# Optimization experiments

Hardware: AMD Instinct MI355X
Metric: run time of the kernel (lower is better)

## Reference

```python
import jax, jax.numpy as jnp
import numpy as np

EPS = 1e-5
B, CIN, L = 512, 5, 1024   # batch, input channels, msp length == d_model
COUT, A, NB = 32, 13, 5    # CNN branch channels, max_atoms, num_bonds_prediction


def conv1d(x, w, pad, groups=1):
    # x: (N, C, L), w: (O, I/groups, K)
    return jax.lax.conv_general_dilated(
        x, w, window_strides=(1,), padding=[(pad, pad)],
        dimension_numbers=("NCH", "OIH", "NCH"), feature_group_count=groups)


def batchnorm(x, g, b):
    # training-mode BN over (N, L) per channel, as nn.BatchNorm1d in train()
    m = jnp.mean(x, axis=(0, 2), keepdims=True)
    v = jnp.var(x, axis=(0, 2), keepdims=True)
    return (x - m) * jax.lax.rsqrt(v + EPS) * g[None, :, None] + b[None, :, None]


def setup_inputs() -> dict:
    key = jax.random.key(0)
    ks = jax.random.split(key, 16)
    n = jax.random.normal
    inp = {
        "src": n(ks[0], (B, CIN, L), dtype=jnp.float32),
        "mask": jnp.ones((B, A), dtype=bool),
        "max_atoms": A,
        # CNN branch 1 (kernel 5) : depthwise, pointwise, BN, residual 1x1 conv
        "dw1": n(ks[1], (CIN, 1, 5), dtype=jnp.float32) * 0.2,
        "pw1": n(ks[2], (COUT, CIN, 1), dtype=jnp.float32) * 0.2,
        "g1": jnp.ones((COUT,), jnp.float32),
        "be1": jnp.zeros((COUT,), jnp.float32),
        "r1w": n(ks[3], (COUT, CIN, 1), dtype=jnp.float32) * 0.2,
        "r1b": jnp.zeros((COUT,), jnp.float32),
        # CNN branch 2 (kernel 3)
        "dw2": n(ks[4], (CIN, 1, 3), dtype=jnp.float32) * 0.2,
        "pw2": n(ks[5], (COUT, CIN, 1), dtype=jnp.float32) * 0.2,
        "g2": jnp.ones((COUT,), jnp.float32),
        "be2": jnp.zeros((COUT,), jnp.float32),
        "r2w": n(ks[6], (COUT, CIN, 1), dtype=jnp.float32) * 0.2,
        "r2b": jnp.zeros((COUT,), jnp.float32),
        # EdgeClassify2 linears: ll1 (2*COUT -> A), fl (2*L -> NB)
        "ll1w": n(ks[7], (A, 2 * COUT), dtype=jnp.float32) * 0.1,
        "ll1b": jnp.zeros((A,), jnp.float32),
        "flw": n(ks[8], (NB, 2 * L), dtype=jnp.float32) * 0.02,
        "flb": jnp.zeros((NB,), jnp.float32),
    }
    return inp


def reference(src, mask, max_atoms, dw1, pw1, g1, be1, r1w, r1b,
              dw2, pw2, g2, be2, r2w, r2b, ll1w, ll1b, flw, flb):
    # ---- CNN encoder ----
    e1 = jax.nn.relu(batchnorm(conv1d(conv1d(src, dw1, 2, groups=CIN), pw1, 0), g1, be1))
    e1 = e1 * (conv1d(src, r1w, 0) + r1b[None, :, None])
    e2 = jax.nn.relu(batchnorm(conv1d(conv1d(src, dw2, 1, groups=CIN), pw2, 0), g2, be2))
    e2 = e2 * (conv1d(src, r2w, 0) + r2b[None, :, None])
    x = jnp.concatenate([e1, e2], axis=1)          # (B, 2*COUT, L)
    # ---- EdgeClassify2 ----
    # ll1 over channel dim: (B, 2*COUT, L) -> (B, A, L)
    h = jnp.einsum("bcl,ac->bal", x, ll1w) + ll1b[None, :, None]
    # vectorized replacement of the O(A^2) python loop:
    # final_e[:, i, j] = concat(h[:, min(i,j)], h[:, max(i,j)])
    idx = jnp.arange(max_atoms)
    mn = jnp.minimum(idx[:, None], idx[None, :])   # (A, A)
    mx = jnp.maximum(idx[:, None], idx[None, :])
    final_e = jnp.concatenate([h[:, mn, :], h[:, mx, :]], axis=-1)  # (B, A, A, 2L)
    out = jnp.einsum("bijd,nd->bijn", final_e, flw) + flb           # (B, A, A, NB)
    return out
```

## Files before the change

### kernel.cpp

```cpp
#include <hip/hip_runtime.h>
#include <hip/hip_bf16.h>

#define BB 512
#define LL 1024
#define AA 13
#define NBP 5
#define NTOT (BB * LL)
#define EPSV 1e-5f

#define WS_F     192
#define WS_PART  256
#define WS_CONST 10496
#define WS_S     16384

typedef __attribute__((ext_vector_type(8))) short bhalf8;
typedef __attribute__((ext_vector_type(4))) float floatx4;

__device__ __forceinline__ unsigned int pk_bf16(float a, float b) {
    __hip_bfloat162 h = __float22bfloat162_rn(make_float2(a, b));
    union { __hip_bfloat162 h2; unsigned int u; } cv; cv.h2 = h;
    return cv.u;
}

template<int CTRL, int RM, bool BC>
__device__ __forceinline__ float dppadd(float v) {
    int t = __builtin_amdgcn_update_dpp(0, __float_as_int(v), CTRL, RM, 0xf, BC);
    return v + __int_as_float(t);
}
__device__ __forceinline__ float wave_sum(float v) {
    v = dppadd<0x111, 0xf, true >(v);
    v = dppadd<0x112, 0xf, true >(v);
    v = dppadd<0x114, 0xf, true >(v);
    v = dppadd<0x118, 0xf, true >(v);
    v = dppadd<0x142, 0xa, false>(v);
    v = dppadd<0x143, 0xc, false>(v);
    return v;
}

__global__ __launch_bounds__(256) void k_moments(
    const float* __restrict__ src,
    const float* __restrict__ dw1,
    const float* __restrict__ dw2,
    const float* __restrict__ flw,
    float* __restrict__ ws)
{
    __shared__ float red[4][40];
    __shared__ float fred[4];
    int tid = threadIdx.x;
    int gid = blockIdx.x * 256 + tid;
    int b = gid >> 7, L0 = (gid & 127) << 3;
    const float* sb = src + b * (5 * LL);

    float w1[5][5], w2[5][3];
#pragma unroll
    for (int c = 0; c < 5; c++) {
#pragma unroll
        for (int t = 0; t < 5; t++) w1[c][t] = dw1[c*5+t];
#pragma unroll
        for (int t = 0; t < 3; t++) w2[c][t] = dw2[c*3+t];
    }

    float x[5][16];
#pragma unroll
    for (int c5 = 0; c5 < 5; c5++) {
        const float* sp = sb + c5 * LL;
        float4 xa = (L0 >= 4)    ? *(const float4*)(sp + L0 - 4) : make_float4(0,0,0,0);
        float4 xb = *(const float4*)(sp + L0);
        float4 xc = *(const float4*)(sp + L0 + 4);
        float4 xd = (L0 <= 1012) ? *(const float4*)(sp + L0 + 8) : make_float4(0,0,0,0);
        x[c5][0]=xa.x; x[c5][1]=xa.y; x[c5][2]=xa.z; x[c5][3]=xa.w;
        x[c5][4]=xb.x; x[c5][5]=xb.y; x[c5][6]=xb.z; x[c5][7]=xb.w;
        x[c5][8]=xc.x; x[c5][9]=xc.y; x[c5][10]=xc.z; x[c5][11]=xc.w;
        x[c5][12]=xd.x; x[c5][13]=xd.y; x[c5][14]=xd.z; x[c5][15]=xd.w;
    }

    float acc[40];
#pragma unroll
    for (int k = 0; k < 40; k++) acc[k] = 0.f;

#pragma unroll
    for (int k = 0; k < 8; k++) {
        float d1[5], d2[5];
#pragma unroll
        for (int c5 = 0; c5 < 5; c5++) {
            d1[c5] = w1[c5][0]*x[c5][k+2] + w1[c5][1]*x[c5][k+3] + w1[c5][2]*x[c5][k+4]
                   + w1[c5][3]*x[c5][k+5] + w1[c5][4]*x[c5][k+6];
            d2[c5] = w2[c5][0]*x[c5][k+3] + w2[c5][1]*x[c5][k+4] + w2[c5][2]*x[c5][k+5];
        }
#pragma unroll
        for (int j = 0; j < 5; j++) { acc[j] += d1[j]; acc[20+j] += d2[j]; }
#pragma unroll
        for (int j = 0; j < 5; j++)
#pragma unroll
            for (int kk = j; kk < 5; kk++) {
                int idx = j*(11-j)/2 + (kk - j);
                acc[5+idx]  += d1[j]*d1[kk];
                acc[25+idx] += d2[j]*d2[kk];
            }
    }

    int lane = tid & 63, wv = tid >> 6;
#pragma unroll
    for (int k = 0; k < 40; k++) acc[k] = wave_sum(acc[k]);
    if (lane == 63) {
#pragma unroll
        for (int k = 0; k < 40; k++) red[wv][k] = acc[k];
    }
    __syncthreads();
    if (tid < 40) {
        ws[WS_PART + blockIdx.x * 40 + tid] =
            red[0][tid] + red[1][tid] + red[2][tid] + red[3][tid];
    }

    if (blockIdx.x < 10) {
        int nn = blockIdx.x;
        int n = nn < 5 ? nn : nn - 5;
        int off = nn < 5 ? 0 : LL;
        float4 v = *(const float4*)(flw + n * (2*LL) + off + tid * 4);
        float s = wave_sum(v.x + v.y + v.z + v.w);
        if (lane == 63) fred[wv] = s;
        __syncthreads();
        if (tid == 0) ws[WS_F + nn] = fred[0] + fred[1] + fred[2] + fred[3];
    }
}

__global__ __launch_bounds__(320) void k_prep(
    float* __restrict__ ws,
    const float* __restrict__ pw1, const float* __restrict__ pw2,
    const float* __restrict__ g1,  const float* __restrict__ be1,
    const float* __restrict__ g2,  const float* __restrict__ be2,
    const float* __restrict__ r1w, const float* __restrict__ r2w,
    const float* __restrict__ r1b, const float* __restrict__ r2b)
{
    __shared__ float momS[40];
    int tid = threadIdx.x;
    {
        int k = tid >> 3, sub = tid & 7;
        float v = 0.f;
#pragma unroll 8
        for (int t2 = 0; t2 < 32; t2++) v += ws[WS_PART + (sub + (t2 << 3)) * 40 + k];
        v += __shfl_xor(v, 1, 64);
        v += __shfl_xor(v, 2, 64);
        v += __shfl_xor(v, 4, 64);
        if (sub == 0) momS[k] = v;
    }
    __syncthreads();
    if (tid < 64) {
        int brc = tid >> 5, o = tid & 31;
        const float invN = 1.0f / (float)NTOT;
        const float* pw = brc ? pw2 : pw1;
        const float* rw = brc ? r2w : r1w;
        const float* s  = momS + (brc ? 20 : 0);
        const float* M  = momS + (brc ? 25 : 5);
        float pwv[5], rwv[5], md[5];
#pragma unroll
        for (int j = 0; j < 5; j++) { pwv[j] = pw[o*5+j]; rwv[j] = rw[o*5+j]; md[j] = s[j] * invN; }
        float meanY = 0.f;
#pragma unroll
        for (int j = 0; j < 5; j++) meanY += pwv[j] * md[j];
        float ey2 = 0.f;
#pragma unroll
        for (int j = 0; j < 5; j++)
#pragma unroll
            for (int k = 0; k < 5; k++) {
                int lo = j < k ? j : k, hi = j < k ? k : j;
                int idx = lo*(11-lo)/2 + (hi - lo);
                ey2 += pwv[j] * pwv[k] * (M[idx] * invN);
            }
        float varY = ey2 - meanY * meanY;
        if (varY < 0.f) varY = 0.f;
        float gg = brc ? g2[o] : g1[o];
        float bb = brc ? be2[o] : be1[o];
        float rb = brc ? r2b[o] : r1b[o];
        float sc = gg * rsqrtf(varY + EPSV);
        float sh = bb - meanY * sc;
        float* dst = ws + WS_CONST + tid * 16;
        dst[0] = pwv[0]*sc; dst[1] = pwv[1]*sc; dst[2] = pwv[2]*sc; dst[3] = pwv[3]*sc;
        dst[4] = pwv[4]*sc; dst[5] = sh;        dst[6] = rb;        dst[7] = 0.f;
        dst[8] = rwv[0];    dst[9] = rwv[1];    dst[10] = rwv[2];   dst[11] = rwv[3];
        dst[12] = rwv[4];   dst[13] = 0.f;      dst[14] = 0.f;      dst[15] = 0.f;
    }
}

__global__ __launch_bounds__(512, 4) void k_fused(
    const float* __restrict__ src,
    const float* __restrict__ dw1,
    const float* __restrict__ dw2,
    const float* __restrict__ flw,
    const float* __restrict__ ws_ro,
    float* __restrict__ ws)
{
    __shared__ __align__(16) unsigned int eBuf[8192];

    int tid = threadIdx.x, bb = blockIdx.x;
    int b = bb >> 1, h = bb & 1;
    int lane = tid & 63;
    int gu = __builtin_amdgcn_readfirstlane(tid >> 6);
    int br = gu >> 2;
    int c0 = gu << 3;

    const float* srcB = src + b * (5 * LL);

    float wdw[5][5];
    if (br == 0) {
#pragma unroll
        for (int c5 = 0; c5 < 5; c5++)
#pragma unroll
            for (int t = 0; t < 5; t++) wdw[c5][t] = dw1[c5*5+t];
    } else {
#pragma unroll
        for (int c5 = 0; c5 < 5; c5++) {
            wdw[c5][0] = 0.f;
            wdw[c5][1] = dw2[c5*3+0]; wdw[c5][2] = dw2[c5*3+1]; wdw[c5][3] = dw2[c5*3+2];
            wdw[c5][4] = 0.f;
        }
    }
    const float* cb = ws_ro + WS_CONST + (c0 << 4);

    int mt   = gu & 3;
    int kgrp = gu >> 2;
    floatx4 Cacc = {0.f, 0.f, 0.f, 0.f};

    int nB = lane & 15;
    int kg = (lane >> 4) << 3;
    const float* fbase = flw + (nB % 5) * 2048 + (nB / 5) * 1024;

    char* eb = (char*)eBuf;

#pragma unroll 1
    for (int p = 0; p < 4; ++p) {
        float fv[2][8];
        {
            int gl0 = (h << 9) + (p << 7) + (kgrp << 6) + kg;
            if (nB < 10) {
                float4 a0 = *(const float4*)(fbase + gl0);
                float4 a1 = *(const float4*)(fbase + gl0 + 4);
                float4 b0 = *(const float4*)(fbase + gl0 + 32);
                float4 b1 = *(const float4*)(fbase + gl0 + 36);
                fv[0][0]=a0.x; fv[0][1]=a0.y; fv[0][2]=a0.z; fv[0][3]=a0.w;
                fv[0][4]=a1.x; fv[0][5]=a1.y; fv[0][6]=a1.z; fv[0][7]=a1.w;
                fv[1][0]=b0.x; fv[1][1]=b0.y; fv[1][2]=b0.z; fv[1][3]=b0.w;
                fv[1][4]=b1.x; fv[1][5]=b1.y; fv[1][6]=b1.z; fv[1][7]=b1.w;
            } else {
#pragma unroll
                for (int j = 0; j < 8; j++) { fv[0][j] = 0.f; fv[1][j] = 0.f; }
            }
        }

        int l0 = (h << 9) + (p << 7) + (lane << 1);
        float dv[5][2], sv[5][2];
#pragma unroll
        for (int c5 = 0; c5 < 5; c5++) {
            const float* s5 = srcB + (c5 << 10);
            float2 xa = (l0 >= 2)    ? *(const float2*)(s5 + l0 - 2) : make_float2(0.f, 0.f);
            float2 xb = *(const float2*)(s5 + l0);
            float2 xc = (l0 <= 1020) ? *(const float2*)(s5 + l0 + 2) : make_float2(0.f, 0.f);
            float xx[6] = {xa.x, xa.y, xb.x, xb.y, xc.x, xc.y};
            sv[c5][0] = xb.x; sv[c5][1] = xb.y;
            if (br == 0) {
#pragma unroll
                for (int q = 0; q < 2; q++)
                    dv[c5][q] = wdw[c5][0]*xx[q] + wdw[c5][1]*xx[q+1] + wdw[c5][2]*xx[q+2]
                              + wdw[c5][3]*xx[q+3] + wdw[c5][4]*xx[q+4];
            } else {
#pragma unroll
                for (int q = 0; q < 2; q++)
                    dv[c5][q] = wdw[c5][1]*xx[q+1] + wdw[c5][2]*xx[q+2] + wdw[c5][3]*xx[q+3];
            }
        }

        int wcol = lane << 2;
#pragma unroll
        for (int ci = 0; ci < 8; ci++) {
            const float4 A  = *(const float4*)(cb + ci*16);
            const float4 B2 = *(const float4*)(cb + ci*16 + 4);
            const float4 R0 = *(const float4*)(cb + ci*16 + 8);
            const float4 R1 = *(const float4*)(cb + ci*16 + 12);
            float e[2];
#pragma unroll
            for (int q = 0; q < 2; q++) {
                float y = B2.y + A.x*dv[0][q] + A.y*dv[1][q] + A.z*dv[2][q]
                                + A.w*dv[3][q] + B2.x*dv[4][q];
                float r = B2.z + R0.x*sv[0][q] + R0.y*sv[1][q] + R0.z*sv[2][q]
                                + R0.w*sv[3][q] + R1.x*sv[4][q];
                e[q] = fmaxf(y, 0.f) * r;
            }
            unsigned int hp = pk_bf16(e[0], e[1]);
            float hi0 = __uint_as_float(hp << 16);
            float hi1 = __uint_as_float(hp & 0xFFFF0000u);
            unsigned int lp = pk_bf16(e[0] - hi0, e[1] - hi1);
            int c = c0 + ci;
            int off = (c << 8) + (wcol ^ ((c & 7) << 4));
            *(unsigned int*)(eb + off)         = hp;
            *(unsigned int*)(eb + 16384 + off) = lp;
        }
        __syncthreads();

        {
            int arow = (mt << 4) + (lane & 15);
            int swz  = (arow & 7) << 4;
            int rb2  = arow << 8;
            bhalf8 bH[2], bL[2];
#pragma unroll
            for (int kk = 0; kk < 2; kk++) {
                union { unsigned int u[4]; bhalf8 v; } uh, ul;
#pragma unroll
                for (int j = 0; j < 4; j++) {
                    float f0 = fv[kk][2*j], f1 = fv[kk][2*j+1];
                    unsigned int hp = pk_bf16(f0, f1);
                    float hi0 = __uint_as_float(hp << 16);
                    float hi1 = __uint_as_float(hp & 0xFFFF0000u);
                    uh.u[j] = hp;
                    ul.u[j] = pk_bf16(f0 - hi0, f1 - hi1);
                }
                bH[kk] = uh.v; bL[kk] = ul.v;
            }
#pragma unroll
            for (int kk = 0; kk < 2; kk++) {
                int kbyte = (((kgrp << 6) + (kk << 5) + kg) << 1) ^ swz;
                bhalf8 aH = *(const bhalf8*)(eb + rb2 + kbyte);
                bhalf8 aL = *(const bhalf8*)(eb + 16384 + rb2 + kbyte);
                Cacc = __builtin_amdgcn_mfma_f32_16x16x32_bf16(aH, bH[kk], Cacc, 0, 0, 0);
                Cacc = __builtin_amdgcn_mfma_f32_16x16x32_bf16(aH, bL[kk], Cacc, 0, 0, 0);
                Cacc = __builtin_amdgcn_mfma_f32_16x16x32_bf16(aL, bH[kk], Cacc, 0, 0, 0);
            }
        }
        __syncthreads();
    }

    {
        float* part = (float*)eBuf;
        int basep = (gu << 8) + ((lane >> 4) << 6) + (lane & 15);
        part[basep]      = Cacc[0];
        part[basep + 16] = Cacc[1];
        part[basep + 32] = Cacc[2];
        part[basep + 48] = Cacc[3];
    }
    __syncthreads();
    for (int idx = tid; idx < 640; idx += 512) {
        int c = idx / 10, n = idx - c * 10;
        int mt2 = c >> 4, row = c & 15;
        const float* part = (const float*)eBuf;
        int o = (row << 4) + n;
        ws[WS_S + bb * 640 + idx] = part[mt2 * 256 + o] + part[(4 + mt2) * 256 + o];
    }
}

__global__ __launch_bounds__(256) void k_out(
    const float* __restrict__ ws,
    const float* __restrict__ ll1w,
    const float* __restrict__ ll1b,
    const float* __restrict__ flb,
    float* __restrict__ out)
{
    __shared__ float llT[832];
    __shared__ float S[640];
    __shared__ float PQ[130];

    int tid = threadIdx.x, b = blockIdx.x;
    for (int idx = tid; idx < 832; idx += 256) {
        int cc = idx / 13, a = idx - cc * 13;
        llT[idx] = ll1w[a * 64 + cc];
    }
    const float* s0 = ws + WS_S + (b * 2) * 640;
    const float* s1 = ws + WS_S + (b * 2 + 1) * 640;
    for (int idx = tid; idx < 640; idx += 256) S[idx] = s0[idx] + s1[idx];
    __syncthreads();

    if (tid < 130) {
        int half = tid >= 65 ? 1 : 0;
        int q = tid - half * 65;
        int a = q / 5, n = q - a * 5;
        int col = half * 5 + n;
        float v = ll1b[a] * ws[WS_F + col];
#pragma unroll 8
        for (int cc = 0; cc < 64; cc++) v += llT[cc * 13 + a] * S[cc * 10 + col];
        PQ[tid] = v;
    }
    __syncthreads();

    for (int idx = tid; idx < AA * AA * NBP; idx += 256) {
        int i = idx / 65;
        int rr = idx - i * 65;
        int j = rr / 5, n = rr - j * 5;
        int mn = i < j ? i : j, mx = i < j ? j : i;
        out[b * (AA * AA * NBP) + idx] = PQ[mn * 5 + n] + PQ[65 + mx * 5 + n] + flb[n];
    }
}

extern "C" void kernel_launch(void* const* d_in, const int* in_sizes, int n_in,
                              void* d_out, int out_size, void* d_ws, size_t ws_size,
                              hipStream_t stream) {
    const float* src  = (const float*)d_in[0];
    const float* dw1  = (const float*)d_in[3];
    const float* pw1  = (const float*)d_in[4];
    const float* g1   = (const float*)d_in[5];
    const float* be1  = (const float*)d_in[6];
    const float* r1w  = (const float*)d_in[7];
    const float* r1b  = (const float*)d_in[8];
    const float* dw2  = (const float*)d_in[9];
    const float* pw2  = (const float*)d_in[10];
    const float* g2   = (const float*)d_in[11];
    const float* be2  = (const float*)d_in[12];
    const float* r2w  = (const float*)d_in[13];
    const float* r2b  = (const float*)d_in[14];
    const float* ll1w = (const float*)d_in[15];
    const float* ll1b = (const float*)d_in[16];
    const float* flw  = (const float*)d_in[17];
    const float* flb  = (const float*)d_in[18];
    float* ws  = (float*)d_ws;
    float* out = (float*)d_out;

    k_moments<<<256, 256, 0, stream>>>(src, dw1, dw2, flw, ws);
    k_prep<<<1, 320, 0, stream>>>(ws, pw1, pw2, g1, be1, g2, be2, r1w, r2w, r1b, r2b);
    k_fused<<<BB * 2, 512, 0, stream>>>(src, dw1, dw2, flw, ws, ws);
    k_out<<<BB, 256, 0, stream>>>(ws, ll1w, ll1b, flb, out);
}
```

Baseline: 157.5 us.

## Precompute depthwise conv once into LDS and build MFMA A-operands in registers

The fused kernel now computes both depthwise conv outputs and the source samples once per position into a swizzled shared buffer, behind a single barrier. Each wave then builds its bf16 hi/lo A fragments directly in registers from that buffer, one channel per lane, instead of staging the elementwise products through shared memory with two barriers per iteration. Per-channel constants are loaded once rather than per iteration. In exchange, each lane does eight positions of pointwise work per step with more shared-memory reads, and the work is split differently across waves.

Measured after the change: 142.1 us. -9.8%, faster.

```diff
diff --git a/kernel.cpp b/kernel.cpp
--- a/kernel.cpp
+++ b/kernel.cpp
@@ -190,146 +190,103 @@
     const float* __restrict__ ws_ro,
     float* __restrict__ ws)
 {
-    __shared__ __align__(16) unsigned int eBuf[8192];
+    __shared__ __align__(16) float dvS[9216 + 64];
 
     int tid = threadIdx.x, bb = blockIdx.x;
     int b = bb >> 1, h = bb & 1;
     int lane = tid & 63;
     int gu = __builtin_amdgcn_readfirstlane(tid >> 6);
-    int br = gu >> 2;
-    int c0 = gu << 3;
+    int mt = gu & 3, lq = gu >> 2;
+    int br = mt >> 1;
 
     const float* srcB = src + b * (5 * LL);
-
-    float wdw[5][5];
-    if (br == 0) {
-#pragma unroll
-        for (int c5 = 0; c5 < 5; c5++)
-#pragma unroll
-            for (int t = 0; t < 5; t++) wdw[c5][t] = dw1[c5*5+t];
-    } else {
+    char* base  = (char*)dvS;
+    char* cbase = (char*)(dvS + 8192);
+
+    {
+        int t = tid, lg = (h << 9) + t;
+        int swz = ((t >> 3) & 3) << 4;
+        float d1v[5], d2v[5], s0[5];
 #pragma unroll
         for (int c5 = 0; c5 < 5; c5++) {
-            wdw[c5][0] = 0.f;
-            wdw[c5][1] = dw2[c5*3+0]; wdw[c5][2] = dw2[c5*3+1]; wdw[c5][3] = dw2[c5*3+2];
-            wdw[c5][4] = 0.f;
-        }
-    }
-    const float* cb = ws_ro + WS_CONST + (c0 << 4);
-
-    int mt   = gu & 3;
-    int kgrp = gu >> 2;
-    floatx4 Cacc = {0.f, 0.f, 0.f, 0.f};
+            const float* s5 = srcB + (c5 << 10);
+            float xm2 = (lg >= 2)    ? s5[lg - 2] : 0.f;
+            float xm1 = (lg >= 1)    ? s5[lg - 1] : 0.f;
+            float x0  = s5[lg];
+            float xp1 = (lg <= 1022) ? s5[lg + 1] : 0.f;
+            float xp2 = (lg <= 1021) ? s5[lg + 2] : 0.f;
+            d1v[c5] = dw1[c5*5+0]*xm2 + dw1[c5*5+1]*xm1 + dw1[c5*5+2]*x0
+                    + dw1[c5*5+3]*xp1 + dw1[c5*5+4]*xp2;
+            d2v[c5] = dw2[c5*3+0]*xm1 + dw2[c5*3+1]*x0 + dw2[c5*3+2]*xp1;
+            s0[c5] = x0;
+        }
+        *(float4*)(base + ((((0<<10)+(t<<1)+0) << 4) ^ swz)) = make_float4(d1v[0],d1v[1],d1v[2],d1v[3]);
+        *(float4*)(base + ((((0<<10)+(t<<1)+1) << 4) ^ swz)) = make_float4(d1v[4],s0[0],s0[1],s0[2]);
+        *(float4*)(base + ((((1<<10)+(t<<1)+0) << 4) ^ swz)) = make_float4(d2v[0],d2v[1],d2v[2],d2v[3]);
+        *(float4*)(base + ((((1<<10)+(t<<1)+1) << 4) ^ swz)) = make_float4(d2v[4],s0[0],s0[1],s0[2]);
+        *(float2*)(cbase + (t << 3)) = make_float2(s0[3], s0[4]);
+    }
+    __syncthreads();
+
+    int ch = (mt << 4) + (lane & 15);
+    const float* cf = ws_ro + WS_CONST + (ch << 4);
+    const float4 A  = *(const float4*)cf;
+    const float4 B2 = *(const float4*)(cf + 4);
+    const float4 R0 = *(const float4*)(cf + 8);
+    const float r4w = cf[12];
 
     int nB = lane & 15;
     int kg = (lane >> 4) << 3;
     const float* fbase = flw + (nB % 5) * 2048 + (nB / 5) * 1024;
-
-    char* eb = (char*)eBuf;
+    floatx4 Cacc = {0.f, 0.f, 0.f, 0.f};
 
 #pragma unroll 1
-    for (int p = 0; p < 4; ++p) {
-        float fv[2][8];
-        {
-            int gl0 = (h << 9) + (p << 7) + (kgrp << 6) + kg;
-            if (nB < 10) {
-                float4 a0 = *(const float4*)(fbase + gl0);
-                float4 a1 = *(const float4*)(fbase + gl0 + 4);
-                float4 b0 = *(const float4*)(fbase + gl0 + 32);
-                float4 b1 = *(const float4*)(fbase + gl0 + 36);
-                fv[0][0]=a0.x; fv[0][1]=a0.y; fv[0][2]=a0.z; fv[0][3]=a0.w;
-                fv[0][4]=a1.x; fv[0][5]=a1.y; fv[0][6]=a1.z; fv[0][7]=a1.w;
-                fv[1][0]=b0.x; fv[1][1]=b0.y; fv[1][2]=b0.z; fv[1][3]=b0.w;
-                fv[1][4]=b1.x; fv[1][5]=b1.y; fv[1][6]=b1.z; fv[1][7]=b1.w;
-            } else {
-#pragma unroll
-                for (int j = 0; j < 8; j++) { fv[0][j] = 0.f; fv[1][j] = 0.f; }
-            }
-        }
-
-        int l0 = (h << 9) + (p << 7) + (lane << 1);
-        float dv[5][2], sv[5][2];
-#pragma unroll
-        for (int c5 = 0; c5 < 5; c5++) {
-            const float* s5 = srcB + (c5 << 10);
-            float2 xa = (l0 >= 2)    ? *(const float2*)(s5 + l0 - 2) : make_float2(0.f, 0.f);
-            float2 xb = *(const float2*)(s5 + l0);
-            float2 xc = (l0 <= 1020) ? *(const float2*)(s5 + l0 + 2) : make_float2(0.f, 0.f);
-            float xx[6] = {xa.x, xa.y, xb.x, xb.y, xc.x, xc.y};
-            sv[c5][0] = xb.x; sv[c5][1] = xb.y;
-            if (br == 0) {
-#pragma unroll
-                for (int q = 0; q < 2; q++)
-                    dv[c5][q] = wdw[c5][0]*xx[q] + wdw[c5][1]*xx[q+1] + wdw[c5][2]*xx[q+2]
-                              + wdw[c5][3]*xx[q+3] + wdw[c5][4]*xx[q+4];
-            } else {
-#pragma unroll
-                for (int q = 0; q < 2; q++)
-                    dv[c5][q] = wdw[c5][1]*xx[q+1] + wdw[c5][2]*xx[q+2] + wdw[c5][3]*xx[q+3];
-            }
-        }
-
-        int wcol = lane << 2;
-#pragma unroll
-        for (int ci = 0; ci < 8; ci++) {
-            const float4 A  = *(const float4*)(cb + ci*16);
-            const float4 B2 = *(const float4*)(cb + ci*16 + 4);
-            const float4 R0 = *(const float4*)(cb + ci*16 + 8);
-            const float4 R1 = *(const float4*)(cb + ci*16 + 12);
-            float e[2];
-#pragma unroll
-            for (int q = 0; q < 2; q++) {
-                float y = B2.y + A.x*dv[0][q] + A.y*dv[1][q] + A.z*dv[2][q]
-                                + A.w*dv[3][q] + B2.x*dv[4][q];
-                float r = B2.z + R0.x*sv[0][q] + R0.y*sv[1][q] + R0.z*sv[2][q]
-                                + R0.w*sv[3][q] + R1.x*sv[4][q];
-                e[q] = fmaxf(y, 0.f) * r;
-            }
-            unsigned int hp = pk_bf16(e[0], e[1]);
+    for (int s = 0; s < 8; ++s) {
+        int lb = (lq << 8) + (s << 5) + kg;
+        float4 f0 = make_float4(0,0,0,0), f1 = make_float4(0,0,0,0);
+        if (nB < 10) {
+            f0 = *(const float4*)(fbase + (h << 9) + lb);
+            f1 = *(const float4*)(fbase + (h << 9) + lb + 4);
+        }
+        int sw = ((lb >> 3) & 3) << 4;
+        float e[8];
+#pragma unroll
+        for (int i = 0; i < 8; ++i) {
+            int l = lb + i;
+            const float4 pa = *(const float4*)(base + ((((br<<10)+(l<<1)+0) << 4) ^ sw));
+            const float4 pb = *(const float4*)(base + ((((br<<10)+(l<<1)+1) << 4) ^ sw));
+            const float2 pc = *(const float2*)(cbase + (l << 3));
+            float y = B2.y + A.x*pa.x + A.y*pa.y + A.z*pa.z + A.w*pa.w + B2.x*pb.x;
+            float r = B2.z + R0.x*pb.y + R0.y*pb.z + R0.z*pb.w + R0.w*pc.x + r4w*pc.y;
+            e[i] = fmaxf(y, 0.f) * r;
+        }
+        union { unsigned int u[4]; bhalf8 v; } ah, al;
+#pragma unroll
+        for (int j = 0; j < 4; j++) {
+            unsigned int hp = pk_bf16(e[2*j], e[2*j+1]);
             float hi0 = __uint_as_float(hp << 16);
             float hi1 = __uint_as_float(hp & 0xFFFF0000u);
-            unsigned int lp = pk_bf16(e[0] - hi0, e[1] - hi1);
-            int c = c0 + ci;
-            int off = (c << 8) + (wcol ^ ((c & 7) << 4));
-            *(unsigned int*)(eb + off)         = hp;
-            *(unsigned int*)(eb + 16384 + off) = lp;
-        }
-        __syncthreads();
-
-        {
-            int arow = (mt << 4) + (lane & 15);
-            int swz  = (arow & 7) << 4;
-            int rb2  = arow << 8;
-            bhalf8 bH[2], bL[2];
-#pragma unroll
-            for (int kk = 0; kk < 2; kk++) {
-                union { unsigned int u[4]; bhalf8 v; } uh, ul;
-#pragma unroll
-                for (int j = 0; j < 4; j++) {
-                    float f0 = fv[kk][2*j], f1 = fv[kk][2*j+1];
-                    unsigned int hp = pk_bf16(f0, f1);
-                    float hi0 = __uint_as_float(hp << 16);
-                    float hi1 = __uint_as_float(hp & 0xFFFF0000u);
-                    uh.u[j] = hp;
-                    ul.u[j] = pk_bf16(f0 - hi0, f1 - hi1);
-                }
-                bH[kk] = uh.v; bL[kk] = ul.v;
-            }
-#pragma unroll
-            for (int kk = 0; kk < 2; kk++) {
-                int kbyte = (((kgrp << 6) + (kk << 5) + kg) << 1) ^ swz;
-                bhalf8 aH = *(const bhalf8*)(eb + rb2 + kbyte);
-                bhalf8 aL = *(const bhalf8*)(eb + 16384 + rb2 + kbyte);
-                Cacc = __builtin_amdgcn_mfma_f32_16x16x32_bf16(aH, bH[kk], Cacc, 0, 0, 0);
-                Cacc = __builtin_amdgcn_mfma_f32_16x16x32_bf16(aH, bL[kk], Cacc, 0, 0, 0);
-                Cacc = __builtin_amdgcn_mfma_f32_16x16x32_bf16(aL, bH[kk], Cacc, 0, 0, 0);
-            }
-        }
-        __syncthreads();
-    }
-
+            ah.u[j] = hp;
+            al.u[j] = pk_bf16(e[2*j] - hi0, e[2*j+1] - hi1);
+        }
+        float fb[8] = {f0.x, f0.y, f0.z, f0.w, f1.x, f1.y, f1.z, f1.w};
+        union { unsigned int u[4]; bhalf8 v; } bh, bl;
+#pragma unroll
+        for (int j = 0; j < 4; j++) {
+            unsigned int hp = pk_bf16(fb[2*j], fb[2*j+1]);
+            float hi0 = __uint_as_float(hp << 16);
+            float hi1 = __uint_as_float(hp & 0xFFFF0000u);
+            bh.u[j] = hp;
+            bl.u[j] = pk_bf16(fb[2*j] - hi0, fb[2*j+1] - hi1);
+        }
+        Cacc = __builtin_amdgcn_mfma_f32_16x16x32_bf16(ah.v, bh.v, Cacc, 0, 0, 0);
+        Cacc = __builtin_amdgcn_mfma_f32_16x16x32_bf16(ah.v, bl.v, Cacc, 0, 0, 0);
+        Cacc = __builtin_amdgcn_mfma_f32_16x16x32_bf16(al.v, bh.v, Cacc, 0, 0, 0);
+    }
+
+    __syncthreads();
     {
-        float* part = (float*)eBuf;
+        float* part = dvS;
         int basep = (gu << 8) + ((lane >> 4) << 6) + (lane & 15);
         part[basep]      = Cacc[0];
         part[basep + 16] = Cacc[1];
@@ -339,9 +296,9 @@
     __syncthreads();
     for (int idx = tid; idx < 640; idx += 512) {
         int c = idx / 10, n = idx - c * 10;
-        int mt2 = c >> 4, row = c & 15;
-        const float* part = (const float*)eBuf;
-        int o = (row << 4) + n;
+        int mt2 = c >> 4, m = c & 15;
+        const float* part = (const float*)dvS;
+        int o = (m << 4) + n;
         ws[WS_S + bb * 640 + idx] = part[mt2 * 256 + o] + part[(4 + mt2) * 256 + o];
     }
 }
```
